# Kernel tuning notes

Measured on AMD Instinct MI355X. Metric: run time of the kernel, lower is better.

The kernel has to match this reference:

```python
import jax, jax.numpy as jnp
import numpy as np

N, K, M, F = 131072, 32, 65536, 64  # queries, neighbors, table rows, alpha channels


def setup_inputs() -> dict:
    key = jax.random.key(0)
    k1, k2, k3 = jax.random.split(key, 3)
    d = jax.random.uniform(k1, (N, K), dtype=jnp.float32)          # squared knn distances
    i = jax.random.randint(k2, (N, K), 0, M)                        # knn indices into alpha
    alpha = jax.random.normal(k3, (M, F), dtype=jnp.float32)        # learned coefficients
    sigma = jnp.ones((1,), dtype=jnp.float32)                       # kernel lengthscale
    return {"d": d, "i": i, "alpha": alpha, "sigma": sigma}


def reference(d, i, alpha, sigma):
    # torch: sum(alpha_[i].permute(2,0,1) * exp(-0.5*d/sigma**2), dim=2) -> [F, N]
    w = jnp.exp(-0.5 * d / (sigma[0] ** 2))          # [N, K] Gaussian weights
    gathered = jnp.take(alpha, i, axis=0)            # [N, K, F] irregular gather
    return jnp.einsum('nkf,nk->fn', gathered, w)     # weighted sum over neighbors -> [F, N]
```

## Files before the change

### kernel.cpp

```cpp
#include <hip/hip_runtime.h>
#include <hip/hip_fp16.h>


#define N_Q    131072
#define K_NB   32
#define F_CH   64
#define M_ROWS 65536

__global__ __launch_bounds__(256) void cvt_alpha_f16(
    const float* __restrict__ alpha, __half* __restrict__ a16)
{
    const int t = blockIdx.x * 256 + threadIdx.x;
    const float4 v0 = ((const float4*)alpha)[(size_t)t * 2 + 0];
    const float4 v1 = ((const float4*)alpha)[(size_t)t * 2 + 1];
    union { __half2 h2[4]; uint4 u; } pk;
    pk.h2[0] = __floats2half2_rn(v0.x, v0.y);
    pk.h2[1] = __floats2half2_rn(v0.z, v0.w);
    pk.h2[2] = __floats2half2_rn(v1.x, v1.y);
    pk.h2[3] = __floats2half2_rn(v1.z, v1.w);
    ((uint4*)a16)[t] = pk.u;
}

__global__ __launch_bounds__(512) void knn_exp_fused3(
    const float*  __restrict__ dmat,
    const int*    __restrict__ imat,
    const __half* __restrict__ a16,
    const float*  __restrict__ sigma,
    float*        __restrict__ out)
{
    __shared__ float    tile[64][65];
    __shared__ unsigned sortbuf[8][8][32];

    const int lane = threadIdx.x & 63;
    const int wave = threadIdx.x >> 6;
    const int n0   = blockIdx.x * 64;
    const bool hi  = (lane >= 32);
    const unsigned lane2 = (unsigned)lane * 2;

    const float s = sigma[0];
    const float c = -0.5f / (s * s);

    const int nbase = n0 + wave * 8;
    const char* pbase = hi
        ? (const char*)&imat[(size_t)nbase * K_NB + (lane - 32)]
        : (const char*)&dmat[(size_t)nbase * K_NB + lane];
    unsigned raw[8];
    #pragma unroll
    for (int qi = 0; qi < 8; ++qi)
        raw[qi] = __builtin_nontemporal_load(
            (const unsigned*)(pbase + (size_t)qi * (K_NB * 4)));

    __builtin_amdgcn_sched_barrier(0);

    #pragma unroll
    for (int qi = 0; qi < 8; ++qi) {
        const float wv = __expf(c * __uint_as_float(raw[qi]));
        const int   iv = (int)raw[qi];

        const unsigned hbits = (unsigned)__half_as_ushort(__float2half_rn(wv));
        const unsigned hb    = (unsigned)__shfl((int)hbits, lane & 31);

        const int quart = (iv >> 14) & 3;
        const unsigned long long m0 = __ballot(hi && quart == 0);
        const unsigned long long m1 = __ballot(hi && quart == 1);
        const unsigned long long m2 = __ballot(hi && quart == 2);
        const unsigned long long m3 = __ballot(hi && quart == 3);
        const int b1 = __popcll(m0);
        const int b2 = b1 + __popcll(m1);
        const int b3 = b2 + __popcll(m2);
        const unsigned long long mq =
            (quart == 0) ? m0 : (quart == 1) ? m1 : (quart == 2) ? m2 : m3;
        const int bq =
            (quart == 0) ? 0 : (quart == 1) ? b1 : (quart == 2) ? b2 : b3;
        const unsigned long long below = (1ull << lane) - 1ull;
        const int pos = bq + __popcll(mq & below);

        if (hi)
            sortbuf[wave][qi][pos] = ((unsigned)iv << 16) | (hb & 0xFFFFu);
    }

    unsigned pv[8];
    float    acc[8];
    #pragma unroll
    for (int qi = 0; qi < 8; ++qi) {
        pv[qi]  = sortbuf[wave][qi][lane & 31];
        acc[qi] = 0.0f;
    }

    #pragma unroll
    for (int p = 0; p < 4; ++p) {
        #pragma unroll
        for (int qi = 0; qi < 8; ++qi) {
            #pragma unroll
            for (int j = 0; j < 8; ++j) {
                const unsigned pk = (unsigned)__builtin_amdgcn_readlane(
                    (int)pv[qi], p * 8 + j);
                __half_raw hr; hr.x = (unsigned short)(pk & 0xFFFFu);
                const float w = __half2float(__half(hr));
                const unsigned off = ((pk >> 16) << 7) + lane2;
                const __half av = *(const __half*)((const char*)a16 + off);
                acc[qi] = fmaf(w, __half2float(av), acc[qi]);
            }
        }
    }

    #pragma unroll
    for (int qi = 0; qi < 8; ++qi)
        tile[wave * 8 + qi][lane] = acc[qi];

    __syncthreads();

    #pragma unroll
    for (int fi = 0; fi < 8; ++fi) {
        const int f = wave * 8 + fi;
        __builtin_nontemporal_store(tile[lane][f],
                                    &out[(size_t)f * N_Q + n0 + lane]);
    }
}

__global__ __launch_bounds__(256) void knn_exp_f32(
    const float* __restrict__ dmat,
    const int*   __restrict__ imat,
    const float* __restrict__ alpha,
    const float* __restrict__ sigma,
    float*       __restrict__ out)
{
    __shared__ float tile[64][65];
    const int lane = threadIdx.x & 63;
    const int wave = threadIdx.x >> 6;
    const int n0   = blockIdx.x * 64;
    const float s = sigma[0];
    const float c = -0.5f / (s * s);

    for (int qi = 0; qi < 16; ++qi) {
        const int q = wave * 16 + qi;
        const int n = n0 + q;
        float wv = 0.0f;
        int   iv = 0;
        if (lane < 32) {
            wv = __expf(c * dmat[(size_t)n * K_NB + lane]);
        } else {
            iv = imat[(size_t)n * K_NB + (lane - 32)];
        }
        float acc = 0.0f;
        #pragma unroll
        for (int k = 0; k < K_NB; ++k) {
            const float wk = __int_as_float(
                __builtin_amdgcn_readlane(__float_as_int(wv), k));
            const int   ik = __builtin_amdgcn_readlane(iv, 32 + k);
            acc = fmaf(wk, alpha[(size_t)ik * F_CH + lane], acc);
        }
        tile[q][lane] = acc;
    }
    __syncthreads();
    #pragma unroll
    for (int fi = 0; fi < 16; ++fi) {
        const int f = wave * 16 + fi;
        out[(size_t)f * N_Q + n0 + lane] = tile[lane][f];
    }
}

extern "C" void kernel_launch(void* const* d_in, const int* in_sizes, int n_in,
                              void* d_out, int out_size, void* d_ws, size_t ws_size,
                              hipStream_t stream) {
    const float* dmat  = (const float*)d_in[0];
    const int*   imat  = (const int*)d_in[1];
    const float* alpha = (const float*)d_in[2];
    const float* sigma = (const float*)d_in[3];
    float* out = (float*)d_out;

    const size_t bytes_a16 = (size_t)M_ROWS * F_CH * sizeof(__half);

    if (ws_size >= bytes_a16) {
        __half* a16 = (__half*)d_ws;
        hipLaunchKernelGGL(cvt_alpha_f16, dim3(M_ROWS * F_CH / 8 / 256),
                           dim3(256), 0, stream, alpha, a16);
        hipLaunchKernelGGL(knn_exp_fused3, dim3(N_Q / 64), dim3(512), 0,
                           stream, dmat, imat, a16, sigma, out);
    } else {
        hipLaunchKernelGGL(knn_exp_f32, dim3(N_Q / 64), dim3(256), 0, stream,
                           dmat, imat, alpha, sigma, out);
    }
}
```

Measured before the change: 61.73 us.

## Quantize alpha rows to int8 with per-row scales folded into gather weights

Replaces the fp16 copy of the alpha table with per-row symmetric int8 quantization plus a float scale per row. The scale is gathered per neighbor and multiplied into the half-precision weight before packing, so the inner gather reads one byte per channel instead of two. The aim is to halve gather traffic and the table footprint so it fits better in cache. In exchange it adds a quantization pass, a scattered scale load, and a much larger accuracy loss than fp16, which may break tolerance.

```diff
diff --git a/kernel.cpp b/kernel.cpp
--- a/kernel.cpp
+++ b/kernel.cpp
@@ -7,26 +7,31 @@
 #define F_CH   64
 #define M_ROWS 65536
 
-__global__ __launch_bounds__(256) void cvt_alpha_f16(
-    const float* __restrict__ alpha, __half* __restrict__ a16)
+__global__ __launch_bounds__(256) void quant_rows(
+    const float* __restrict__ alpha,
+    signed char* __restrict__ a8,
+    float*       __restrict__ scale)
 {
-    const int t = blockIdx.x * 256 + threadIdx.x;
-    const float4 v0 = ((const float4*)alpha)[(size_t)t * 2 + 0];
-    const float4 v1 = ((const float4*)alpha)[(size_t)t * 2 + 1];
-    union { __half2 h2[4]; uint4 u; } pk;
-    pk.h2[0] = __floats2half2_rn(v0.x, v0.y);
-    pk.h2[1] = __floats2half2_rn(v0.z, v0.w);
-    pk.h2[2] = __floats2half2_rn(v1.x, v1.y);
-    pk.h2[3] = __floats2half2_rn(v1.z, v1.w);
-    ((uint4*)a16)[t] = pk.u;
+    const int lane = threadIdx.x & 63;
+    const int row  = (blockIdx.x << 2) + (threadIdx.x >> 6);
+
+    const float v = __builtin_nontemporal_load(&alpha[(size_t)row * F_CH + lane]);
+    float m = fabsf(v);
+    #pragma unroll
+    for (int off = 32; off; off >>= 1) m = fmaxf(m, __shfl_xor(m, off));
+
+    const float inv = (m > 0.0f) ? (127.0f / m) : 0.0f;
+    a8[(size_t)row * F_CH + lane] = (signed char)(int)rintf(v * inv);
+    if (lane == 0) scale[row] = m * (1.0f / 127.0f);
 }
 
-__global__ __launch_bounds__(512) void knn_exp_fused3(
-    const float*  __restrict__ dmat,
-    const int*    __restrict__ imat,
-    const __half* __restrict__ a16,
-    const float*  __restrict__ sigma,
-    float*        __restrict__ out)
+__global__ __launch_bounds__(512) void knn_exp_i8_phased(
+    const float*       __restrict__ dmat,
+    const int*         __restrict__ imat,
+    const signed char* __restrict__ a8,
+    const float*       __restrict__ scale,
+    const float*       __restrict__ sigma,
+    float*             __restrict__ out)
 {
     __shared__ float    tile[64][65];
     __shared__ unsigned sortbuf[8][8][32];
@@ -35,7 +40,6 @@
     const int wave = threadIdx.x >> 6;
     const int n0   = blockIdx.x * 64;
     const bool hi  = (lane >= 32);
-    const unsigned lane2 = (unsigned)lane * 2;
 
     const float s = sigma[0];
     const float c = -0.5f / (s * s);
@@ -52,13 +56,21 @@
 
     __builtin_amdgcn_sched_barrier(0);
 
+    float srow[8];
+    #pragma unroll
+    for (int qi = 0; qi < 8; ++qi)
+        srow[qi] = scale[raw[qi] & 0xFFFFu];
+
+    __builtin_amdgcn_sched_barrier(0);
+
     #pragma unroll
     for (int qi = 0; qi < 8; ++qi) {
         const float wv = __expf(c * __uint_as_float(raw[qi]));
         const int   iv = (int)raw[qi];
 
-        const unsigned hbits = (unsigned)__half_as_ushort(__float2half_rn(wv));
-        const unsigned hb    = (unsigned)__shfl((int)hbits, lane & 31);
+        const float wp = __shfl(wv, lane & 31);
+        const unsigned hb = (unsigned)__half_as_ushort(
+            __float2half_rn(wp * srow[qi]));
 
         const int quart = (iv >> 14) & 3;
         const unsigned long long m0 = __ballot(hi && quart == 0);
@@ -97,9 +109,10 @@
                     (int)pv[qi], p * 8 + j);
                 __half_raw hr; hr.x = (unsigned short)(pk & 0xFFFFu);
                 const float w = __half2float(__half(hr));
-                const unsigned off = ((pk >> 16) << 7) + lane2;
-                const __half av = *(const __half*)((const char*)a16 + off);
-                acc[qi] = fmaf(w, __half2float(av), acc[qi]);
+                const unsigned off = (pk >> 16) << 6;
+                const signed char q =
+                    *(const signed char*)((const char*)a8 + off + lane);
+                acc[qi] = fmaf(w, (float)q, acc[qi]);
             }
         }
     }
@@ -169,14 +182,16 @@
     const float* sigma = (const float*)d_in[3];
     float* out = (float*)d_out;
 
-    const size_t bytes_a16 = (size_t)M_ROWS * F_CH * sizeof(__half);
+    const size_t bytes_a8    = (size_t)M_ROWS * F_CH;
+    const size_t bytes_scale = (size_t)M_ROWS * sizeof(float);
 
-    if (ws_size >= bytes_a16) {
-        __half* a16 = (__half*)d_ws;
-        hipLaunchKernelGGL(cvt_alpha_f16, dim3(M_ROWS * F_CH / 8 / 256),
-                           dim3(256), 0, stream, alpha, a16);
-        hipLaunchKernelGGL(knn_exp_fused3, dim3(N_Q / 64), dim3(512), 0,
-                           stream, dmat, imat, a16, sigma, out);
+    if (ws_size >= bytes_a8 + bytes_scale) {
+        signed char* a8  = (signed char*)d_ws;
+        float*       scl = (float*)((char*)d_ws + bytes_a8);
+        hipLaunchKernelGGL(quant_rows, dim3(M_ROWS / 4), dim3(256), 0, stream,
+                           alpha, a8, scl);
+        hipLaunchKernelGGL(knn_exp_i8_phased, dim3(N_Q / 64), dim3(512), 0,
+                           stream, dmat, imat, a8, scl, sigma, out);
     } else {
         hipLaunchKernelGGL(knn_exp_f32, dim3(N_Q / 64), dim3(256), 0, stream,
                            dmat, imat, alpha, sigma, out);
```

New measurement: 88.81 us. 43.9% more time.
